# Kernel tuning notes

Measured on AMD Instinct MI355X. Metric: run time of the kernel, lower is better.

## Reference

```python
import jax, jax.numpy as jnp
import numpy as np

B, N, M = 2, 10000, 320000
F, LAT, STY = 64, 128, 128
HEADS, HID = 4, 32
OUT = 3 + F  # 67
NEG = 0.2    # leaky relu slope (both activation and GAT attention)
EPS = 1e-5


def leaky(x):
    return jax.nn.leaky_relu(x, NEG)


def layer_norm(x, g, b):
    mu = jnp.mean(x, axis=-1, keepdims=True)
    var = jnp.var(x, axis=-1, keepdims=True)
    return (x - mu) * jax.lax.rsqrt(var + EPS) * g + b


def gat_conv(h, src, dst, W, a_src, a_dst, bias, heads, out_dim, n_nodes, concat):
    # h: [n, in]; W: [in, heads*out_dim]; a_*: [heads, out_dim]
    ht = (h @ W).reshape(n_nodes, heads, out_dim)
    al_s = jnp.einsum('nhd,hd->nh', ht, a_src)  # source contribution
    al_d = jnp.einsum('nhd,hd->nh', ht, a_dst)  # destination contribution
    e = leaky(al_s[src] + al_d[dst])            # [E, heads]
    emax = jax.ops.segment_max(e, dst, num_segments=n_nodes)
    ex = jnp.exp(e - emax[dst])
    denom = jax.ops.segment_sum(ex, dst, num_segments=n_nodes)
    alpha = ex / (denom[dst] + 1e-16)           # scatter-softmax over in-edges
    msg = ht[src] * alpha[:, :, None]           # [E, heads, out_dim]
    agg = jax.ops.segment_sum(msg, dst, num_segments=n_nodes)
    agg = agg.reshape(n_nodes, heads * out_dim) if concat else agg.mean(axis=1)
    return agg + bias


def setup_inputs():
    key = jax.random.key(0)
    ks = jax.random.split(key, 20)
    g = lambda i, sh, s=0.05: jax.random.normal(ks[i], sh, jnp.float32) * s
    d = {}
    d['z'] = g(0, (B, LAT), 1.0)
    d['x'] = g(1, (N, F), 1.0)
    d['pos'] = g(2, (N, 3), 1.0)
    d['edge_index'] = jax.random.randint(ks[3], (2, M), 0, N)
    d['w1'] = g(4, (LAT, 256)); d['b1'] = jnp.zeros((256,), jnp.float32)
    d['w2'] = g(5, (256, 512)); d['b2'] = jnp.zeros((512,), jnp.float32)
    d['w3'] = g(6, (512, STY)); d['b3'] = jnp.zeros((STY,), jnp.float32)
    in0 = F + STY
    d['gw0'] = g(7, (in0, HEADS * HID)); d['ga0s'] = g(8, (HEADS, HID)); d['ga0d'] = g(9, (HEADS, HID)); d['gb0'] = jnp.zeros((HEADS * HID,), jnp.float32)
    in1 = HEADS * HID
    d['gw1'] = g(10, (in1, HEADS * HID)); d['ga1s'] = g(11, (HEADS, HID)); d['ga1d'] = g(12, (HEADS, HID)); d['gb1'] = jnp.zeros((HEADS * HID,), jnp.float32)
    d['gw2'] = g(13, (in1, OUT)); d['ga2s'] = g(14, (1, OUT)); d['ga2d'] = g(15, (1, OUT)); d['gb2'] = jnp.zeros((OUT,), jnp.float32)
    d['ln0_g'] = jnp.ones((in1,), jnp.float32); d['ln0_b'] = jnp.zeros((in1,), jnp.float32)
    d['ln1_g'] = jnp.ones((in1,), jnp.float32); d['ln1_b'] = jnp.zeros((in1,), jnp.float32)
    return d


def _batched_edges(edge_index):
    # replicate template edges B times with node-id offsets, then add self-loops
    ei = jnp.concatenate([edge_index + b * N for b in range(B)], axis=1)
    sl = jnp.arange(B * N, dtype=edge_index.dtype)
    src = jnp.concatenate([ei[0], sl])
    dst = jnp.concatenate([ei[1], sl])
    return src, dst


def _forward(z, x, pos, src, dst,
             w1, b1, w2, b2, w3, b3,
             gw0, ga0s, ga0d, gb0, gw1, ga1s, ga1d, gb1, gw2, ga2s, ga2d, gb2,
             ln0_g, ln0_b, ln1_g, ln1_b):
    n_tot = B * N
    # style MLP
    s = leaky(z @ w1 + b1)
    s = leaky(s @ w2 + b2)
    style = s @ w3 + b3                               # [B, STY]
    xb = jnp.tile(x, (B, 1))                          # [B*N, F]
    pb = jnp.tile(pos, (B, 1))                        # [B*N, 3]
    style_exp = jnp.repeat(style, N, axis=0)          # [B*N, STY]
    H = jnp.concatenate([xb, style_exp], axis=1)
    H = gat_conv(H, src, dst, gw0, ga0s, ga0d, gb0, HEADS, HID, n_tot, True)
    H = leaky(layer_norm(H, ln0_g, ln0_b))
    H = gat_conv(H, src, dst, gw1, ga1s, ga1d, gb1, HEADS, HID, n_tot, True)
    H = leaky(layer_norm(H, ln1_g, ln1_b))
    H_out = gat_conv(H, src, dst, gw2, ga2s, ga2d, gb2, 1, OUT, n_tot, False)
    p_new = pb + H_out[:, :3]
    f_new = xb + H_out[:, 3:]
    return f_new, p_new


def reference(z, x, pos, edge_index,
              w1, b1, w2, b2, w3, b3,
              gw0, ga0s, ga0d, gb0, gw1, ga1s, ga1d, gb1, gw2, ga2s, ga2d, gb2,
              ln0_g, ln0_b, ln1_g, ln1_b):
    src, dst = _batched_edges(edge_index)
    return _forward(z, x, pos, src, dst,
                    w1, b1, w2, b2, w3, b3,
                    gw0, ga0s, ga0d, gb0, gw1, ga1s, ga1d, gb1, gw2, ga2s, ga2d, gb2,
                    ln0_g, ln0_b, ln1_g, ln1_b)
```

## Files before the change

kernel.cpp:

```cpp
#include <hip/hip_runtime.h>
#include <hip/hip_bf16.h>

#define DEV_INLINE __device__ __forceinline__

constexpr int Nn   = 10000;
constexpr int NT   = 20000;
constexpr int Me   = 320000;
constexpr int STRIDE = 96;
constexpr float NEG = 0.2f;

typedef float  f32x4  __attribute__((ext_vector_type(4)));
typedef float  f32x2  __attribute__((ext_vector_type(2)));
typedef short  bf16x8 __attribute__((ext_vector_type(8)));

DEV_INLINE float leaky(float x){ return x >= 0.f ? x : NEG*x; }

DEV_INLINE ushort f2bf(float v){
  __hip_bfloat16 h = __float2bfloat16(v);
  return *reinterpret_cast<ushort*>(&h);
}
DEV_INLINE float bf2f(ushort u){
  uint x = ((uint)u) << 16;
  return __uint_as_float(x);
}

DEV_INLINE unsigned char f2f8(float v){
#if __has_builtin(__builtin_amdgcn_cvt_pk_fp8_f32)
  return (unsigned char)(__builtin_amdgcn_cvt_pk_fp8_f32(v, v, 0, false) & 0xFF);
#else
  uint u = __float_as_uint(v);
  uint s = (u >> 24) & 0x80u;
  uint au = u & 0x7FFFFFFFu;
  if (au >= 0x43E00000u) return (unsigned char)(s | 0x7Eu);
  uint au2 = au + 0x0007FFFFu + ((au >> 20) & 1u);
  int e = (int)(au2 >> 23) - 120;
  if (e <= 0) return (unsigned char)s;
  uint r = ((uint)e << 3) | ((au2 >> 20) & 7u);
  if (r >= 0x7Fu) r = 0x7Eu;
  return (unsigned char)(s | r);
#endif
}
template<bool HI>
DEV_INLINE f32x2 f8x2f(uint p){
#if __has_builtin(__builtin_amdgcn_cvt_pk_f32_fp8)
  return __builtin_amdgcn_cvt_pk_f32_fp8((int)p, HI);
#else
  uint b0 = HI ? ((p >> 16) & 0xFFu) : (p & 0xFFu);
  uint b1 = HI ? ((p >> 24) & 0xFFu) : ((p >> 8) & 0xFFu);
  f32x2 r;
  uint m0 = b0 & 0x7Fu, m1 = b1 & 0x7Fu;
  uint f0 = (m0 >= 8) ? ((m0 + 960u) << 20) : 0u;
  uint f1 = (m1 >= 8) ? ((m1 + 960u) << 20) : 0u;
  f0 |= (b0 & 0x80u) << 24; f1 |= (b1 & 0x80u) << 24;
  r.x = __uint_as_float(f0); r.y = __uint_as_float(f1);
  return r;
#endif
}

DEV_INLINE float sel4(float4 w, int h){
  return h < 2 ? (h == 0 ? w.x : w.y) : (h == 2 ? w.z : w.w);
}
DEV_INLINE float red16(float v){
  v += __shfl_xor(v, 1); v += __shfl_xor(v, 2);
  v += __shfl_xor(v, 4); v += __shfl_xor(v, 8);
  return v;
}
DEV_INLINE float red32(float v){
  v += __shfl_xor(v, 1); v += __shfl_xor(v, 2);
  v += __shfl_xor(v, 4); v += __shfl_xor(v, 8);
  v += __shfl_xor(v, 16);
  return v;
}

template<int K>
__global__ __launch_bounds__(256) void k_mlp(const float* __restrict__ in,
    const float* __restrict__ W, const float* __restrict__ bias,
    float* __restrict__ out, int OD, int doAct, int mlpBlocks,
    int* __restrict__ zbuf, int zn, int zblk,
    const float* __restrict__ w3, const float* __restrict__ G,
    float* __restrict__ M, const float* __restrict__ b3, float* __restrict__ bG,
    int mblk){
  if ((int)blockIdx.x >= mlpBlocks){
    int b2 = blockIdx.x - mlpBlocks;
    if (b2 < zblk){
      int i = b2*256 + threadIdx.x;
      if (i < zn) zbuf[i] = 0;
    } else if ((b2 -= zblk) < mblk){
      int k = b2*2 + (threadIdx.x >> 7);
      int j = threadIdx.x & 127;
      float a = 0.f;
      for (int m=0; m<128; m++) a += w3[k*128 + m] * G[m*128 + j];
      M[(size_t)k*128 + j] = a;
    } else {
      if (threadIdx.x < 128){
        int j = threadIdx.x;
        float a = 0.f;
        for (int m=0; m<128; m++) a += b3[m] * G[m*128 + j];
        bG[j] = a;
      }
    }
    return;
  }
  int wave = threadIdx.x >> 6, lane = threadIdx.x & 63;
  int o = blockIdx.x*4 + wave;
  if (o >= 2*OD) return;
  int b = (o >= OD) ? 1 : 0;
  int j = o - b*OD;
  const float* __restrict__ ip = in + b*K;
  float acc = 0.f;
  #pragma unroll 2
  for (int k = lane; k < K; k += 64) acc += ip[k] * W[(size_t)k*OD + j];
  #pragma unroll
  for (int off = 32; off; off >>= 1) acc += __shfl_xor(acc, off);
  if (lane == 0){
    float v = acc + (bias ? bias[j] : 0.f);
    out[o] = doAct ? leaky(v) : v;
  }
}

__global__ __launch_bounds__(256) void k_ht0_mfma(const float* __restrict__ x,
    const float* __restrict__ gw0, const float* __restrict__ styleW0,
    const float* __restrict__ a_s, const float* __restrict__ a_d,
    unsigned char* __restrict__ ht0, float* __restrict__ alS, float* __restrict__ alD,
    int mbBlocks, const int* __restrict__ eidx, int* __restrict__ cnt,
    ushort* __restrict__ slot){
  if ((int)blockIdx.x >= mbBlocks){
    int e = (blockIdx.x - mbBlocks)*256 + threadIdx.x;
    if (e < Me){
      int s = eidx[e], d = eidx[Me + e];
      int p = atomicAdd(&cnt[d], 1);
      if (p < STRIDE) slot[(size_t)d*STRIDE + p] = (ushort)s;
    }
    return;
  }
  __shared__ ushort bt[128*64];
  __shared__ float stycS[2][4], stycD[2][4];
  int t = threadIdx.x;
  int lane = t & 63, l15 = lane & 15, g = lane >> 4;
  int wid = t >> 6;
  int mbase = blockIdx.x*128 + wid*32;

  bf16x8 afr[2][2];
  #pragma unroll
  for (int mf=0; mf<2; mf++){
    int row = mbase + mf*16 + l15;
    int rc = row < Nn ? row : Nn-1;
    const float* xp = x + (size_t)rc*64 + g*8;
    #pragma unroll
    for (int ks=0; ks<2; ks++){
      float4 va = *(const float4*)(xp + ks*32);
      float4 vb = *(const float4*)(xp + ks*32 + 4);
      bf16x8 f;
      f[0] = (short)f2bf(va.x); f[1] = (short)f2bf(va.y);
      f[2] = (short)f2bf(va.z); f[3] = (short)f2bf(va.w);
      f[4] = (short)f2bf(vb.x); f[5] = (short)f2bf(vb.y);
      f[6] = (short)f2bf(vb.z); f[7] = (short)f2bf(vb.w);
      afr[mf][ks] = f;
    }
  }

  for (int idx = t; idx < 64*128; idx += 256){
    int k = idx >> 7, c = idx & 127;
    uint byte = ((uint)(c*64 + k) << 1) ^ ((uint)(c&7) << 4);
    *(ushort*)((char*)bt + byte) = f2bf(gw0[k*128 + c]);
  }

  if (t < 128){
    int c = t, h = c >> 5;
    float as_c = a_s[c], ad_c = a_d[c];
    float s0 = styleW0[c], s1 = styleW0[128 + c];
    float v0s = red32(s0*as_c), v0d = red32(s0*ad_c);
    float v1s = red32(s1*as_c), v1d = red32(s1*ad_c);
    if ((lane & 31) == 0){
      stycS[0][h] = v0s; stycD[0][h] = v0d;
      stycS[1][h] = v1s; stycD[1][h] = v1d;
    }
  }
  __syncthreads();

  f32x4 acc[2][8];
  #pragma unroll
  for (int mf=0; mf<2; mf++)
    #pragma unroll
    for (int nf=0; nf<8; nf++) acc[mf][nf] = (f32x4){0.f,0.f,0.f,0.f};

  #pragma unroll
  for (int ks=0; ks<2; ks++){
    int kb = ks*32 + g*8;
    bf16x8 bfr[8];
    #pragma unroll
    for (int nf=0; nf<8; nf++){
      int c = nf*16 + l15;
      uint byte = ((uint)(c*64 + kb) << 1) ^ ((uint)(c&7) << 4);
      bfr[nf] = *(const bf16x8*)((const char*)bt + byte);
    }
    #pragma unroll
    for (int mf=0; mf<2; mf++)
      #pragma unroll
      for (int nf=0; nf<8; nf++)
        acc[mf][nf] = __builtin_amdgcn_mfma_f32_16x16x32_bf16(
            afr[mf][ks], bfr[nf], acc[mf][nf], 0, 0, 0);
  }

  float sw0[8], sw1[8], as_v[8], ad_v[8];
  #pragma unroll
  for (int nf=0; nf<8; nf++){
    int c = nf*16 + l15;
    sw0[nf] = styleW0[c]; sw1[nf] = styleW0[128 + c];
    as_v[nf] = a_s[c];    ad_v[nf] = a_d[c];
  }
  #pragma unroll
  for (int mf=0; mf<2; mf++){
    int rbase = mbase + mf*16 + g*4;
    #pragma unroll
    for (int r=0; r<4; r++){
      int row = rbase + r;
      bool ok = (row < Nn);
      #pragma unroll
      for (int nf=0; nf<8; nf++){
        int c = nf*16 + l15;
        if (ok){
          float v = acc[mf][nf][r];
          ht0[(size_t)row*128 + c]      = f2f8(v + sw0[nf]);
          ht0[(size_t)(Nn+row)*128 + c] = f2f8(v + sw1[nf]);
        }
      }
      float ps0 = acc[mf][0][r]*as_v[0] + acc[mf][1][r]*as_v[1];
      float ps1 = acc[mf][2][r]*as_v[2] + acc[mf][3][r]*as_v[3];
      float ps2 = acc[mf][4][r]*as_v[4] + acc[mf][5][r]*as_v[5];
      float ps3 = acc[mf][6][r]*as_v[6] + acc[mf][7][r]*as_v[7];
      float pd0 = acc[mf][0][r]*ad_v[0] + acc[mf][1][r]*ad_v[1];
      float pd1 = acc[mf][2][r]*ad_v[2] + acc[mf][3][r]*ad_v[3];
      float pd2 = acc[mf][4][r]*ad_v[4] + acc[mf][5][r]*ad_v[5];
      float pd3 = acc[mf][6][r]*ad_v[6] + acc[mf][7][r]*ad_v[7];
      ps0 = red16(ps0); ps1 = red16(ps1); ps2 = red16(ps2); ps3 = red16(ps3);
      pd0 = red16(pd0); pd1 = red16(pd1); pd2 = red16(pd2); pd3 = red16(pd3);
      if (l15 == 0 && ok){
        *(float4*)(alS + (size_t)row*4) = make_float4(
            ps0 + stycS[0][0], ps1 + stycS[0][1], ps2 + stycS[0][2], ps3 + stycS[0][3]);
        *(float4*)(alD + (size_t)row*4) = make_float4(
            pd0 + stycD[0][0], pd1 + stycD[0][1], pd2 + stycD[0][2], pd3 + stycD[0][3]);
        *(float4*)(alS + (size_t)(Nn+row)*4) = make_float4(
            ps0 + stycS[1][0], ps1 + stycS[1][1], ps2 + stycS[1][2], ps3 + stycS[1][3]);
        *(float4*)(alD + (size_t)(Nn+row)*4) = make_float4(
            pd0 + stycD[1][0], pd1 + stycD[1][1], pd2 + stycD[1][2], pd3 + stycD[1][3]);
      }
    }
  }
}

template<int NCOL, int LDO, int NF, int NHEAD>
__global__ __launch_bounds__(256) void k_mm_mfma(const ushort* __restrict__ A,
    const float* __restrict__ W, unsigned char* __restrict__ out,
    const float* __restrict__ a_s, const float* __restrict__ a_d,
    float* __restrict__ alS, float* __restrict__ alD, int M){
  constexpr int NCOLP = NF*16;
  __shared__ ushort bt[NCOLP*128];
  int t = threadIdx.x;
  int wid = t >> 6, lane = t & 63, l15 = lane & 15, g = lane >> 4;
  int mbase = blockIdx.x*128 + wid*32;

  bf16x8 afr[2][4];
  #pragma unroll
  for (int mf=0; mf<2; mf++){
    int row = mbase + mf*16 + l15;
    int rc = row < M ? row : M-1;
    const ushort* ap = A + (size_t)rc*128 + g*8;
    #pragma unroll
    for (int ks=0; ks<4; ks++)
      afr[mf][ks] = *(const bf16x8*)(ap + ks*32);
  }

  for (int idx = t; idx < 128*NCOLP; idx += 256){
    int k = idx / NCOLP, c = idx % NCOLP;
    float v = (c < NCOL) ? W[k*NCOL + c] : 0.f;
    uint byte = ((uint)(c*128 + k) << 1) ^ ((uint)(c&7) << 4);
    *(ushort*)((char*)bt + byte) = f2bf(v);
  }
  __syncthreads();

  f32x4 acc[2][NF];
  #pragma unroll
  for (int mf=0; mf<2; mf++)
    #pragma unroll
    for (int nf=0; nf<NF; nf++) acc[mf][nf] = (f32x4){0.f,0.f,0.f,0.f};

  #pragma unroll
  for (int ks=0; ks<4; ks++){
    int kb = ks*32 + g*8;
    bf16x8 bfr[NF];
    #pragma unroll
    for (int nf=0; nf<NF; nf++){
      int c = nf*16 + l15;
      uint byte = ((uint)(c*128 + kb) << 1) ^ ((uint)(c&7) << 4);
      bfr[nf] = *(const bf16x8*)((const char*)bt + byte);
    }
    #pragma unroll
    for (int mf=0; mf<2; mf++)
      #pragma unroll
      for (int nf=0; nf<NF; nf++)
        acc[mf][nf] = __builtin_amdgcn_mfma_f32_16x16x32_bf16(
            afr[mf][ks], bfr[nf], acc[mf][nf], 0, 0, 0);
  }

  #pragma unroll
  for (int mf=0; mf<2; mf++){
    int rbase = mbase + mf*16 + g*4;
    #pragma unroll
    for (int nf=0; nf<NF; nf++){
      int c = nf*16 + l15;
      if (c < LDO){
        #pragma unroll
        for (int r=0; r<4; r++){
          int row = rbase + r;
          if (row < M) out[(size_t)row*LDO + c] =
              (c < NCOL) ? f2f8(acc[mf][nf][r]) : (unsigned char)0;
        }
      }
    }
  }

  float as_v[NF], ad_v[NF];
  #pragma unroll
  for (int nf=0; nf<NF; nf++){
    int c = nf*16 + l15;
    as_v[nf] = (c < NCOL) ? a_s[c] : 0.f;
    ad_v[nf] = (c < NCOL) ? a_d[c] : 0.f;
  }
  #pragma unroll
  for (int mf=0; mf<2; mf++){
    #pragma unroll
    for (int r=0; r<4; r++){
      int row = mbase + mf*16 + g*4 + r;
      if constexpr (NHEAD == 4){
        float ps0 = acc[mf][0][r]*as_v[0] + acc[mf][1][r]*as_v[1];
        float ps1 = acc[mf][2][r]*as_v[2] + acc[mf][3][r]*as_v[3];
        float ps2 = acc[mf][4][r]*as_v[4] + acc[mf][5][r]*as_v[5];
        float ps3 = acc[mf][6][r]*as_v[6] + acc[mf][7][r]*as_v[7];
        float pd0 = acc[mf][0][r]*ad_v[0] + acc[mf][1][r]*ad_v[1];
        float pd1 = acc[mf][2][r]*ad_v[2] + acc[mf][3][r]*ad_v[3];
        float pd2 = acc[mf][4][r]*ad_v[4] + acc[mf][5][r]*ad_v[5];
        float pd3 = acc[mf][6][r]*ad_v[6] + acc[mf][7][r]*ad_v[7];
        ps0 = red16(ps0); ps1 = red16(ps1); ps2 = red16(ps2); ps3 = red16(ps3);
        pd0 = red16(pd0); pd1 = red16(pd1); pd2 = red16(pd2); pd3 = red16(pd3);
        if (l15 == 0 && row < M){
          *(float4*)(alS + (size_t)row*4) = make_float4(ps0, ps1, ps2, ps3);
          *(float4*)(alD + (size_t)row*4) = make_float4(pd0, pd1, pd2, pd3);
        }
      } else {
        float ps = 0.f, pd = 0.f;
        #pragma unroll
        for (int nf=0; nf<NF; nf++){
          ps += acc[mf][nf][r]*as_v[nf];
          pd += acc[mf][nf][r]*ad_v[nf];
        }
        ps = red16(ps); pd = red16(pd);
        if (l15 == 0 && row < M){
          alS[row] = ps; alD[row] = pd;
        }
      }
    }
  }
}

__global__ __launch_bounds__(256) void k_gat128(const unsigned char* __restrict__ ht,
    const float* __restrict__ alS, const float* __restrict__ alD,
    const int* __restrict__ deg, const ushort* __restrict__ slot,
    const float* __restrict__ gb, const float* __restrict__ lng,
    const float* __restrict__ lnb, ushort* __restrict__ outH, int n){
  __shared__ float wbuf[4][4][68];
  __shared__ int   sbuf[4][64];
  int wave = threadIdx.x >> 6, lane = threadIdx.x & 63;
  int dd = blockIdx.x*4 + wave;
  if (dd >= n) return;
  int tr  = (dd >= Nn) ? dd - Nn : dd;
  int off = (dd >= Nn) ? Nn : 0;
  int sub = lane >> 5, li = lane & 31;
  int c0 = li*4;
  int h  = li >> 3;
  float4 ald4 = *(const float4*)(alD + dd*4);
  int dg = deg[tr]; if (dg > STRIDE) dg = STRIDE;
  int begin = tr*STRIDE, end = begin + dg;

  float4 asl = *(const float4*)(alS + dd*4);
  float4 wsl;
  wsl.x = __expf(leaky(asl.x + ald4.x));
  wsl.y = __expf(leaky(asl.y + ald4.y));
  wsl.z = __expf(leaky(asl.z + ald4.z));
  wsl.w = __expf(leaky(asl.w + ald4.w));
  float es = sel4(wsl, h);
  float acc0=0.f, acc1=0.f, acc2=0.f, acc3=0.f, den=0.f;
  if (sub == 0){
    uint sv = *(const uint*)(ht + (size_t)dd*128 + c0);
    f32x2 lo = f8x2f<false>(sv), hi = f8x2f<true>(sv);
    den = es;
    acc0 = es * lo.x; acc1 = es * lo.y;
    acc2 = es * hi.x; acc3 = es * hi.y;
  }

  const unsigned char* __restrict__ htp = ht + c0;

  for (int j = begin; j < end; j += 64){
    int nc = min(64, end - j);
    if (lane < nc){
      int s = (int)slot[j + lane] + off;
      float4 as4 = *(const float4*)(alS + s*4);
      wbuf[wave][0][lane] = __expf(leaky(as4.x + ald4.x));
      wbuf[wave][1][lane] = __expf(leaky(as4.y + ald4.y));
      wbuf[wave][2][lane] = __expf(leaky(as4.z + ald4.z));
      wbuf[wave][3][lane] = __expf(leaky(as4.w + ald4.w));
      sbuf[wave][lane] = s;
    }
    const float* __restrict__ wh = wbuf[wave][h];
    int q = 0;
    for (; q + 8 <= nc; q += 8){
      int sv[4]; float wv[4];
      #pragma unroll
      for (int u=0;u<4;u++){ int e = q + 2*u + sub; sv[u] = sbuf[wave][e]; wv[u] = wh[e]; }
      uint hv[4];
      #pragma unroll
      for (int u=0;u<4;u++) hv[u] = *(const uint*)(htp + (size_t)sv[u]*128);
      #pragma unroll
      for (int u=0;u<4;u++){
        f32x2 lo = f8x2f<false>(hv[u]), hi = f8x2f<true>(hv[u]);
        den  += wv[u];
        acc0 += wv[u] * lo.x; acc1 += wv[u] * lo.y;
        acc2 += wv[u] * hi.x; acc3 += wv[u] * hi.y;
      }
    }
    for (; q < nc; q += 2){
      int e = q + sub;
      if (e < nc){
        int s = sbuf[wave][e];
        float w = wh[e];
        uint hv = *(const uint*)(htp + (size_t)s*128);
        f32x2 lo = f8x2f<false>(hv), hi = f8x2f<true>(hv);
        den  += w;
        acc0 += w * lo.x; acc1 += w * lo.y;
        acc2 += w * hi.x; acc3 += w * hi.y;
      }
    }
  }
  acc0 += __shfl_xor(acc0, 32); acc1 += __shfl_xor(acc1, 32);
  acc2 += __shfl_xor(acc2, 32); acc3 += __shfl_xor(acc3, 32);
  den  += __shfl_xor(den, 32);

  float idn = 1.f / (den + 1e-16f);
  float4 gbv = *(const float4*)(gb + c0);
  float v0 = acc0*idn + gbv.x;
  float v1 = acc1*idn + gbv.y;
  float v2 = acc2*idn + gbv.z;
  float v3 = acc3*idn + gbv.w;

  float sum = v0+v1+v2+v3;
  float sq  = v0*v0+v1*v1+v2*v2+v3*v3;
  sum = red32(sum); sq = red32(sq);
  float mu  = sum * (1.f/128.f);
  float var = sq  * (1.f/128.f) - mu*mu;
  float inv = rsqrtf(var + 1e-5f);
  float4 lg = *(const float4*)(lng + c0);
  float4 lb = *(const float4*)(lnb + c0);
  if (sub == 0){
    float y0 = (v0 - mu)*inv*lg.x + lb.x;
    float y1 = (v1 - mu)*inv*lg.y + lb.y;
    float y2 = (v2 - mu)*inv*lg.z + lb.z;
    float y3 = (v3 - mu)*inv*lg.w + lb.w;
    uint2 ow;
    ow.x = (uint)f2bf(leaky(y0)) | ((uint)f2bf(leaky(y1)) << 16);
    ow.y = (uint)f2bf(leaky(y2)) | ((uint)f2bf(leaky(y3)) << 16);
    *(uint2*)(outH + (size_t)dd*128 + c0) = ow;
  }
}

__global__ __launch_bounds__(256) void k_gat_out(const unsigned char* __restrict__ ht2,
    const float* __restrict__ alS, const float* __restrict__ alD,
    const int* __restrict__ deg, const ushort* __restrict__ slot,
    const float* __restrict__ gb2, const float* __restrict__ x,
    const float* __restrict__ pos, float* __restrict__ out, int n){
  __shared__ float wbuf[4][64];
  __shared__ int   sbuf[4][64];
  int wave = threadIdx.x >> 6, lane = threadIdx.x & 63;
  int dd = blockIdx.x*4 + wave;
  if (dd >= n) return;
  int tr  = (dd >= Nn) ? dd - Nn : dd;
  int off = (dd >= Nn) ? Nn : 0;
  int c0 = lane*2;
  bool act = (c0 < 67);
  float ald = alD[dd];
  int dg = deg[tr]; if (dg > STRIDE) dg = STRIDE;
  int begin = tr*STRIDE, end = begin + dg;

  float wsl = __expf(leaky(alS[dd] + ald));
  float den  = wsl;
  uint sv0 = act ? (uint)*(const ushort*)(ht2 + (size_t)dd*68 + c0) : 0u;
  f32x2 sd = f8x2f<false>(sv0);
  float acc0 = wsl * sd.x;
  float acc1 = wsl * sd.y;

  const unsigned char* __restrict__ h2p = ht2 + c0;

  for (int j = begin; j < end; j += 64){
    int nc = min(64, end - j);
    if (lane < nc){
      int s = (int)slot[j + lane] + off;
      wbuf[wave][lane] = __expf(leaky(alS[s] + ald));
      sbuf[wave][lane] = s;
    }
    int q = 0;
    for (; q + 8 <= nc; q += 8){
      int sv[8]; float wv[8];
      #pragma unroll
      for (int u=0;u<8;u++){ sv[u] = sbuf[wave][q+u]; wv[u] = wbuf[wave][q+u]; }
      uint hv[8];
      #pragma unroll
      for (int u=0;u<8;u++) hv[u] = act ? (uint)*(const ushort*)(h2p + (size_t)sv[u]*68) : 0u;
      #pragma unroll
      for (int u=0;u<8;u++){
        f32x2 d = f8x2f<false>(hv[u]);
        den  += wv[u];
        acc0 += wv[u] * d.x;
        acc1 += wv[u] * d.y;
      }
    }
    for (; q < nc; q++){
      int s = sbuf[wave][q]; float w = wbuf[wave][q];
      uint hv = act ? (uint)*(const ushort*)(h2p + (size_t)s*68) : 0u;
      f32x2 d = f8x2f<false>(hv);
      den  += w;
      acc0 += w * d.x;
      acc1 += w * d.y;
    }
  }
  if (!act) return;
  float idn = 1.f / (den + 1e-16f);
  int i = tr;
  int c1 = c0 + 1;
  float v0 = acc0*idn + gb2[c0];
  if (c0 < 3) out[NT*64 + dd*3 + c0] = pos[i*3 + c0] + v0;
  else        out[dd*64 + (c0-3)]    = x[i*64 + (c0-3)] + v0;
  if (c1 < 67){
    float v1 = acc1*idn + gb2[c1];
    if (c1 < 3) out[NT*64 + dd*3 + c1] = pos[i*3 + c1] + v1;
    else        out[dd*64 + (c1-3)]    = x[i*64 + (c1-3)] + v1;
  }
}

extern "C" void kernel_launch(void* const* d_in, const int* in_sizes, int n_in,
                              void* d_out, int out_size, void* d_ws, size_t ws_size,
                              hipStream_t stream){
  const float* z    = (const float*)d_in[0];
  const float* x    = (const float*)d_in[1];
  const float* pos  = (const float*)d_in[2];
  const int*   eidx = (const int*)  d_in[3];
  const float* w1   = (const float*)d_in[4];
  const float* b1   = (const float*)d_in[5];
  const float* w2   = (const float*)d_in[6];
  const float* b2   = (const float*)d_in[7];
  const float* w3   = (const float*)d_in[8];
  const float* b3   = (const float*)d_in[9];
  const float* gw0  = (const float*)d_in[10];
  const float* ga0s = (const float*)d_in[11];
  const float* ga0d = (const float*)d_in[12];
  const float* gb0  = (const float*)d_in[13];
  const float* gw1  = (const float*)d_in[14];
  const float* ga1s = (const float*)d_in[15];
  const float* ga1d = (const float*)d_in[16];
  const float* gb1  = (const float*)d_in[17];
  const float* gw2  = (const float*)d_in[18];
  const float* ga2s = (const float*)d_in[19];
  const float* ga2d = (const float*)d_in[20];
  const float* gb2  = (const float*)d_in[21];
  const float* ln0g = (const float*)d_in[22];
  const float* ln0b = (const float*)d_in[23];
  const float* ln1g = (const float*)d_in[24];
  const float* ln1b = (const float*)d_in[25];
  float* out = (float*)d_out;

  float* ws       = (float*)d_ws;
  float* styleW0  = ws;
  float* s1buf    = ws + 256;
  float* s2buf    = s1buf + 512;
  float* Mbuf     = s2buf + 1024;
  float* bGbuf    = Mbuf + 512*128;
  float* alS      = bGbuf + 128;
  float* alD      = alS + 80000;
  unsigned char* htA = (unsigned char*)(alD + 80000);
  ushort* htB     = (ushort*)(htA + (size_t)NT*128);
  unsigned char* ht2c = (unsigned char*)(htB + (size_t)NT*128);
  int*   cnt      = (int*)(ht2c + (size_t)NT*68);
  ushort* slot    = (ushort*)(cnt + Nn);

  const float* G = gw0 + 64*128;

  const int ZB  = (Nn + 255)/256;
  const int MBk = 256;
  k_mlp<128><<<128 + ZB + MBk + 1, 256, 0, stream>>>(
      z, w1, b1, s1buf, 256, 1, 128,
      cnt, Nn, ZB, w3, G, Mbuf, b3, bGbuf, MBk);
  k_mlp<256><<<256, 256, 0, stream>>>(s1buf, w2, b2, s2buf, 512, 1, 256,
      nullptr, 0, 0, nullptr, nullptr, nullptr, nullptr, nullptr, 0);
  k_mlp<512><<<64, 256, 0, stream>>>(s2buf, Mbuf, bGbuf, styleW0, 128, 0, 64,
      nullptr, 0, 0, nullptr, nullptr, nullptr, nullptr, nullptr, 0);

  const int MB0 = (Nn+127)/128;
  const int EB  = (Me+255)/256;
  k_ht0_mfma<<<MB0 + EB, 256, 0, stream>>>(x, gw0, styleW0, ga0s, ga0d,
                                           htA, alS, alD, MB0, eidx, cnt, slot);
  k_gat128<<<(NT+3)/4, 256, 0, stream>>>(htA, alS, alD, cnt, slot,
                                         gb0, ln0g, ln0b, htB, NT);
  const int MB = (NT+127)/128;
  k_mm_mfma<128,128,8,4><<<MB, 256, 0, stream>>>(htB, gw1, htA, ga1s, ga1d, alS, alD, NT);
  k_gat128<<<(NT+3)/4, 256, 0, stream>>>(htA, alS, alD, cnt, slot,
                                         gb1, ln1g, ln1b, htB, NT);
  k_mm_mfma<67,68,5,1><<<MB, 256, 0, stream>>>(htB, gw2, ht2c, ga2s, ga2d, alS, alD, NT);
  k_gat_out<<<(NT+3)/4, 256, 0, stream>>>(ht2c, alS, alD, cnt, slot,
                                          gb2, x, pos, out, NT);
}
```

Before: 130.3 us.

## Process both batch copies of each node per wave in GAT aggregation kernels

```diff
diff --git a/kernel.cpp b/kernel.cpp
--- a/kernel.cpp
+++ b/kernel.cpp
@@ -367,35 +367,37 @@
     const float* __restrict__ alS, const float* __restrict__ alD,
     const int* __restrict__ deg, const ushort* __restrict__ slot,
     const float* __restrict__ gb, const float* __restrict__ lng,
-    const float* __restrict__ lnb, ushort* __restrict__ outH, int n){
-  __shared__ float wbuf[4][4][68];
+    const float* __restrict__ lnb, ushort* __restrict__ outH){
+  __shared__ float wbuf[4][8][68];
   __shared__ int   sbuf[4][64];
   int wave = threadIdx.x >> 6, lane = threadIdx.x & 63;
-  int dd = blockIdx.x*4 + wave;
-  if (dd >= n) return;
-  int tr  = (dd >= Nn) ? dd - Nn : dd;
-  int off = (dd >= Nn) ? Nn : 0;
+  int tr = blockIdx.x*4 + wave;
+  if (tr >= Nn) return;
   int sub = lane >> 5, li = lane & 31;
   int c0 = li*4;
   int h  = li >> 3;
-  float4 ald4 = *(const float4*)(alD + dd*4);
+  float4 ad0 = *(const float4*)(alD + (size_t)tr*4);
+  float4 ad1 = *(const float4*)(alD + (size_t)(tr+Nn)*4);
   int dg = deg[tr]; if (dg > STRIDE) dg = STRIDE;
   int begin = tr*STRIDE, end = begin + dg;
 
-  float4 asl = *(const float4*)(alS + dd*4);
-  float4 wsl;
-  wsl.x = __expf(leaky(asl.x + ald4.x));
-  wsl.y = __expf(leaky(asl.y + ald4.y));
-  wsl.z = __expf(leaky(asl.z + ald4.z));
-  wsl.w = __expf(leaky(asl.w + ald4.w));
-  float es = sel4(wsl, h);
-  float acc0=0.f, acc1=0.f, acc2=0.f, acc3=0.f, den=0.f;
+  float4 as0 = *(const float4*)(alS + (size_t)tr*4);
+  float4 as1 = *(const float4*)(alS + (size_t)(tr+Nn)*4);
+  float4 w0s, w1s;
+  w0s.x = __expf(leaky(as0.x + ad0.x)); w0s.y = __expf(leaky(as0.y + ad0.y));
+  w0s.z = __expf(leaky(as0.z + ad0.z)); w0s.w = __expf(leaky(as0.w + ad0.w));
+  w1s.x = __expf(leaky(as1.x + ad1.x)); w1s.y = __expf(leaky(as1.y + ad1.y));
+  w1s.z = __expf(leaky(as1.z + ad1.z)); w1s.w = __expf(leaky(as1.w + ad1.w));
+  float e0s = sel4(w0s, h), e1s = sel4(w1s, h);
+  float a00=0,a01=0,a02=0,a03=0,den0=0;
+  float a10=0,a11=0,a12=0,a13=0,den1=0;
   if (sub == 0){
-    uint sv = *(const uint*)(ht + (size_t)dd*128 + c0);
-    f32x2 lo = f8x2f<false>(sv), hi = f8x2f<true>(sv);
-    den = es;
-    acc0 = es * lo.x; acc1 = es * lo.y;
-    acc2 = es * hi.x; acc3 = es * hi.y;
+    uint v0 = *(const uint*)(ht + (size_t)tr*128 + c0);
+    uint v1 = *(const uint*)(ht + (size_t)(tr+Nn)*128 + c0);
+    f32x2 l0 = f8x2f<false>(v0), h0v = f8x2f<true>(v0);
+    f32x2 l1 = f8x2f<false>(v1), h1v = f8x2f<true>(v1);
+    den0 = e0s; a00 = e0s*l0.x; a01 = e0s*l0.y; a02 = e0s*h0v.x; a03 = e0s*h0v.y;
+    den1 = e1s; a10 = e1s*l1.x; a11 = e1s*l1.y; a12 = e1s*h1v.x; a13 = e1s*h1v.y;
   }
 
   const unsigned char* __restrict__ htp = ht + c0;
@@ -403,72 +405,105 @@
   for (int j = begin; j < end; j += 64){
     int nc = min(64, end - j);
     if (lane < nc){
-      int s = (int)slot[j + lane] + off;
-      float4 as4 = *(const float4*)(alS + s*4);
-      wbuf[wave][0][lane] = __expf(leaky(as4.x + ald4.x));
-      wbuf[wave][1][lane] = __expf(leaky(as4.y + ald4.y));
-      wbuf[wave][2][lane] = __expf(leaky(as4.z + ald4.z));
-      wbuf[wave][3][lane] = __expf(leaky(as4.w + ald4.w));
+      int s = (int)slot[j + lane];
+      float4 p0 = *(const float4*)(alS + (size_t)s*4);
+      float4 p1 = *(const float4*)(alS + (size_t)(s+Nn)*4);
+      wbuf[wave][0][lane] = __expf(leaky(p0.x + ad0.x));
+      wbuf[wave][1][lane] = __expf(leaky(p0.y + ad0.y));
+      wbuf[wave][2][lane] = __expf(leaky(p0.z + ad0.z));
+      wbuf[wave][3][lane] = __expf(leaky(p0.w + ad0.w));
+      wbuf[wave][4][lane] = __expf(leaky(p1.x + ad1.x));
+      wbuf[wave][5][lane] = __expf(leaky(p1.y + ad1.y));
+      wbuf[wave][6][lane] = __expf(leaky(p1.z + ad1.z));
+      wbuf[wave][7][lane] = __expf(leaky(p1.w + ad1.w));
       sbuf[wave][lane] = s;
     }
-    const float* __restrict__ wh = wbuf[wave][h];
+    const float* __restrict__ wh0 = wbuf[wave][h];
+    const float* __restrict__ wh1 = wbuf[wave][4+h];
     int q = 0;
     for (; q + 8 <= nc; q += 8){
-      int sv[4]; float wv[4];
-      #pragma unroll
-      for (int u=0;u<4;u++){ int e = q + 2*u + sub; sv[u] = sbuf[wave][e]; wv[u] = wh[e]; }
-      uint hv[4];
-      #pragma unroll
-      for (int u=0;u<4;u++) hv[u] = *(const uint*)(htp + (size_t)sv[u]*128);
+      int sv[4]; float v0[4], v1[4];
+      #pragma unroll
+      for (int u=0;u<4;u++){ int e = q + 2*u + sub; sv[u] = sbuf[wave][e]; v0[u] = wh0[e]; v1[u] = wh1[e]; }
+      uint g0[4], g1[4];
       #pragma unroll
       for (int u=0;u<4;u++){
-        f32x2 lo = f8x2f<false>(hv[u]), hi = f8x2f<true>(hv[u]);
-        den  += wv[u];
-        acc0 += wv[u] * lo.x; acc1 += wv[u] * lo.y;
-        acc2 += wv[u] * hi.x; acc3 += wv[u] * hi.y;
+        g0[u] = *(const uint*)(htp + (size_t)sv[u]*128);
+        g1[u] = *(const uint*)(htp + ((size_t)sv[u]+Nn)*128);
+      }
+      #pragma unroll
+      for (int u=0;u<4;u++){
+        f32x2 lo0 = f8x2f<false>(g0[u]), hi0 = f8x2f<true>(g0[u]);
+        f32x2 lo1 = f8x2f<false>(g1[u]), hi1 = f8x2f<true>(g1[u]);
+        den0 += v0[u];
+        a00 += v0[u]*lo0.x; a01 += v0[u]*lo0.y; a02 += v0[u]*hi0.x; a03 += v0[u]*hi0.y;
+        den1 += v1[u];
+        a10 += v1[u]*lo1.x; a11 += v1[u]*lo1.y; a12 += v1[u]*hi1.x; a13 += v1[u]*hi1.y;
       }
     }
     for (; q < nc; q += 2){
       int e = q + sub;
       if (e < nc){
         int s = sbuf[wave][e];
-        float w = wh[e];
-        uint hv = *(const uint*)(htp + (size_t)s*128);
-        f32x2 lo = f8x2f<false>(hv), hi = f8x2f<true>(hv);
-        den  += w;
-        acc0 += w * lo.x; acc1 += w * lo.y;
-        acc2 += w * hi.x; acc3 += w * hi.y;
-      }
-    }
-  }
-  acc0 += __shfl_xor(acc0, 32); acc1 += __shfl_xor(acc1, 32);
-  acc2 += __shfl_xor(acc2, 32); acc3 += __shfl_xor(acc3, 32);
-  den  += __shfl_xor(den, 32);
-
-  float idn = 1.f / (den + 1e-16f);
+        float v0 = wh0[e], v1 = wh1[e];
+        uint g0 = *(const uint*)(htp + (size_t)s*128);
+        uint g1 = *(const uint*)(htp + ((size_t)s+Nn)*128);
+        f32x2 lo0 = f8x2f<false>(g0), hi0 = f8x2f<true>(g0);
+        f32x2 lo1 = f8x2f<false>(g1), hi1 = f8x2f<true>(g1);
+        den0 += v0; a00 += v0*lo0.x; a01 += v0*lo0.y; a02 += v0*hi0.x; a03 += v0*hi0.y;
+        den1 += v1; a10 += v1*lo1.x; a11 += v1*lo1.y; a12 += v1*hi1.x; a13 += v1*hi1.y;
+      }
+    }
+  }
+  a00 += __shfl_xor(a00, 32); a01 += __shfl_xor(a01, 32);
+  a02 += __shfl_xor(a02, 32); a03 += __shfl_xor(a03, 32);
+  a10 += __shfl_xor(a10, 32); a11 += __shfl_xor(a11, 32);
+  a12 += __shfl_xor(a12, 32); a13 += __shfl_xor(a13, 32);
+  den0 += __shfl_xor(den0, 32); den1 += __shfl_xor(den1, 32);
+
   float4 gbv = *(const float4*)(gb + c0);
-  float v0 = acc0*idn + gbv.x;
-  float v1 = acc1*idn + gbv.y;
-  float v2 = acc2*idn + gbv.z;
-  float v3 = acc3*idn + gbv.w;
-
-  float sum = v0+v1+v2+v3;
-  float sq  = v0*v0+v1*v1+v2*v2+v3*v3;
-  sum = red32(sum); sq = red32(sq);
-  float mu  = sum * (1.f/128.f);
-  float var = sq  * (1.f/128.f) - mu*mu;
-  float inv = rsqrtf(var + 1e-5f);
   float4 lg = *(const float4*)(lng + c0);
   float4 lb = *(const float4*)(lnb + c0);
-  if (sub == 0){
-    float y0 = (v0 - mu)*inv*lg.x + lb.x;
-    float y1 = (v1 - mu)*inv*lg.y + lb.y;
-    float y2 = (v2 - mu)*inv*lg.z + lb.z;
-    float y3 = (v3 - mu)*inv*lg.w + lb.w;
-    uint2 ow;
-    ow.x = (uint)f2bf(leaky(y0)) | ((uint)f2bf(leaky(y1)) << 16);
-    ow.y = (uint)f2bf(leaky(y2)) | ((uint)f2bf(leaky(y3)) << 16);
-    *(uint2*)(outH + (size_t)dd*128 + c0) = ow;
+
+  {
+    float idn = 1.f / (den0 + 1e-16f);
+    float v0 = a00*idn + gbv.x, v1 = a01*idn + gbv.y;
+    float v2 = a02*idn + gbv.z, v3 = a03*idn + gbv.w;
+    float sum = red32(v0+v1+v2+v3);
+    float sq  = red32(v0*v0+v1*v1+v2*v2+v3*v3);
+    float mu  = sum * (1.f/128.f);
+    float var = sq  * (1.f/128.f) - mu*mu;
+    float inv = rsqrtf(var + 1e-5f);
+    if (sub == 0){
+      float y0 = (v0 - mu)*inv*lg.x + lb.x;
+      float y1 = (v1 - mu)*inv*lg.y + lb.y;
+      float y2 = (v2 - mu)*inv*lg.z + lb.z;
+      float y3 = (v3 - mu)*inv*lg.w + lb.w;
+      uint2 ow;
+      ow.x = (uint)f2bf(leaky(y0)) | ((uint)f2bf(leaky(y1)) << 16);
+      ow.y = (uint)f2bf(leaky(y2)) | ((uint)f2bf(leaky(y3)) << 16);
+      *(uint2*)(outH + (size_t)tr*128 + c0) = ow;
+    }
+  }
+  {
+    float idn = 1.f / (den1 + 1e-16f);
+    float v0 = a10*idn + gbv.x, v1 = a11*idn + gbv.y;
+    float v2 = a12*idn + gbv.z, v3 = a13*idn + gbv.w;
+    float sum = red32(v0+v1+v2+v3);
+    float sq  = red32(v0*v0+v1*v1+v2*v2+v3*v3);
+    float mu  = sum * (1.f/128.f);
+    float var = sq  * (1.f/128.f) - mu*mu;
+    float inv = rsqrtf(var + 1e-5f);
+    if (sub == 0){
+      float y0 = (v0 - mu)*inv*lg.x + lb.x;
+      float y1 = (v1 - mu)*inv*lg.y + lb.y;
+      float y2 = (v2 - mu)*inv*lg.z + lb.z;
+      float y3 = (v3 - mu)*inv*lg.w + lb.w;
+      uint2 ow;
+      ow.x = (uint)f2bf(leaky(y0)) | ((uint)f2bf(leaky(y1)) << 16);
+      ow.y = (uint)f2bf(leaky(y2)) | ((uint)f2bf(leaky(y3)) << 16);
+      *(uint2*)(outH + (size_t)(tr+Nn)*128 + c0) = ow;
+    }
   }
 }
 
@@ -476,72 +511,89 @@
     const float* __restrict__ alS, const float* __restrict__ alD,
     const int* __restrict__ deg, const ushort* __restrict__ slot,
     const float* __restrict__ gb2, const float* __restrict__ x,
-    const float* __restrict__ pos, float* __restrict__ out, int n){
-  __shared__ float wbuf[4][64];
+    const float* __restrict__ pos, float* __restrict__ out){
+  __shared__ float wbuf[4][2][64];
   __shared__ int   sbuf[4][64];
   int wave = threadIdx.x >> 6, lane = threadIdx.x & 63;
-  int dd = blockIdx.x*4 + wave;
-  if (dd >= n) return;
-  int tr  = (dd >= Nn) ? dd - Nn : dd;
-  int off = (dd >= Nn) ? Nn : 0;
+  int tr = blockIdx.x*4 + wave;
+  if (tr >= Nn) return;
   int c0 = lane*2;
   bool act = (c0 < 67);
-  float ald = alD[dd];
+  float ald0 = alD[tr], ald1 = alD[tr+Nn];
   int dg = deg[tr]; if (dg > STRIDE) dg = STRIDE;
   int begin = tr*STRIDE, end = begin + dg;
 
-  float wsl = __expf(leaky(alS[dd] + ald));
-  float den  = wsl;
-  uint sv0 = act ? (uint)*(const ushort*)(ht2 + (size_t)dd*68 + c0) : 0u;
-  f32x2 sd = f8x2f<false>(sv0);
-  float acc0 = wsl * sd.x;
-  float acc1 = wsl * sd.y;
+  float w0s = __expf(leaky(alS[tr] + ald0));
+  float w1s = __expf(leaky(alS[tr+Nn] + ald1));
+  float den0 = w0s, den1 = w1s;
+  uint v0i = act ? (uint)*(const ushort*)(ht2 + (size_t)tr*68 + c0) : 0u;
+  uint v1i = act ? (uint)*(const ushort*)(ht2 + (size_t)(tr+Nn)*68 + c0) : 0u;
+  f32x2 s0 = f8x2f<false>(v0i), s1 = f8x2f<false>(v1i);
+  float a00 = w0s*s0.x, a01 = w0s*s0.y;
+  float a10 = w1s*s1.x, a11 = w1s*s1.y;
 
   const unsigned char* __restrict__ h2p = ht2 + c0;
 
   for (int j = begin; j < end; j += 64){
     int nc = min(64, end - j);
     if (lane < nc){
-      int s = (int)slot[j + lane] + off;
-      wbuf[wave][lane] = __expf(leaky(alS[s] + ald));
+      int s = (int)slot[j + lane];
+      wbuf[wave][0][lane] = __expf(leaky(alS[s] + ald0));
+      wbuf[wave][1][lane] = __expf(leaky(alS[s+Nn] + ald1));
       sbuf[wave][lane] = s;
     }
     int q = 0;
-    for (; q + 8 <= nc; q += 8){
-      int sv[8]; float wv[8];
-      #pragma unroll
-      for (int u=0;u<8;u++){ sv[u] = sbuf[wave][q+u]; wv[u] = wbuf[wave][q+u]; }
-      uint hv[8];
-      #pragma unroll
-      for (int u=0;u<8;u++) hv[u] = act ? (uint)*(const ushort*)(h2p + (size_t)sv[u]*68) : 0u;
-      #pragma unroll
-      for (int u=0;u<8;u++){
-        f32x2 d = f8x2f<false>(hv[u]);
-        den  += wv[u];
-        acc0 += wv[u] * d.x;
-        acc1 += wv[u] * d.y;
+    for (; q + 4 <= nc; q += 4){
+      int sv[4]; float v0[4], v1[4];
+      #pragma unroll
+      for (int u=0;u<4;u++){ sv[u] = sbuf[wave][q+u]; v0[u] = wbuf[wave][0][q+u]; v1[u] = wbuf[wave][1][q+u]; }
+      uint g0[4], g1[4];
+      #pragma unroll
+      for (int u=0;u<4;u++){
+        g0[u] = act ? (uint)*(const ushort*)(h2p + (size_t)sv[u]*68) : 0u;
+        g1[u] = act ? (uint)*(const ushort*)(h2p + ((size_t)sv[u]+Nn)*68) : 0u;
+      }
+      #pragma unroll
+      for (int u=0;u<4;u++){
+        f32x2 d0 = f8x2f<false>(g0[u]), d1 = f8x2f<false>(g1[u]);
+        den0 += v0[u]; a00 += v0[u]*d0.x; a01 += v0[u]*d0.y;
+        den1 += v1[u]; a10 += v1[u]*d1.x; a11 += v1[u]*d1.y;
       }
     }
     for (; q < nc; q++){
-      int s = sbuf[wave][q]; float w = wbuf[wave][q];
-      uint hv = act ? (uint)*(const ushort*)(h2p + (size_t)s*68) : 0u;
-      f32x2 d = f8x2f<false>(hv);
-      den  += w;
-      acc0 += w * d.x;
-      acc1 += w * d.y;
+      int s = sbuf[wave][q];
+      float v0 = wbuf[wave][0][q], v1 = wbuf[wave][1][q];
+      uint g0 = act ? (uint)*(const ushort*)(h2p + (size_t)s*68) : 0u;
+      uint g1 = act ? (uint)*(const ushort*)(h2p + ((size_t)s+Nn)*68) : 0u;
+      f32x2 d0 = f8x2f<false>(g0), d1 = f8x2f<false>(g1);
+      den0 += v0; a00 += v0*d0.x; a01 += v0*d0.y;
+      den1 += v1; a10 += v1*d1.x; a11 += v1*d1.y;
     }
   }
   if (!act) return;
-  float idn = 1.f / (den + 1e-16f);
-  int i = tr;
-  int c1 = c0 + 1;
-  float v0 = acc0*idn + gb2[c0];
-  if (c0 < 3) out[NT*64 + dd*3 + c0] = pos[i*3 + c0] + v0;
-  else        out[dd*64 + (c0-3)]    = x[i*64 + (c0-3)] + v0;
-  if (c1 < 67){
-    float v1 = acc1*idn + gb2[c1];
-    if (c1 < 3) out[NT*64 + dd*3 + c1] = pos[i*3 + c1] + v1;
-    else        out[dd*64 + (c1-3)]    = x[i*64 + (c1-3)] + v1;
+  int i = tr, c1 = c0 + 1;
+  {
+    float idn = 1.f / (den0 + 1e-16f);
+    float v0 = a00*idn + gb2[c0];
+    if (c0 < 3) out[NT*64 + tr*3 + c0] = pos[i*3 + c0] + v0;
+    else        out[(size_t)tr*64 + (c0-3)] = x[i*64 + (c0-3)] + v0;
+    if (c1 < 67){
+      float v1 = a01*idn + gb2[c1];
+      if (c1 < 3) out[NT*64 + tr*3 + c1] = pos[i*3 + c1] + v1;
+      else        out[(size_t)tr*64 + (c1-3)] = x[i*64 + (c1-3)] + v1;
+    }
+  }
+  {
+    int dd = tr + Nn;
+    float idn = 1.f / (den1 + 1e-16f);
+    float v0 = a10*idn + gb2[c0];
+    if (c0 < 3) out[NT*64 + dd*3 + c0] = pos[i*3 + c0] + v0;
+    else        out[(size_t)dd*64 + (c0-3)] = x[i*64 + (c0-3)] + v0;
+    if (c1 < 67){
+      float v1 = a11*idn + gb2[c1];
+      if (c1 < 3) out[NT*64 + dd*3 + c1] = pos[i*3 + c1] + v1;
+      else        out[(size_t)dd*64 + (c1-3)] = x[i*64 + (c1-3)] + v1;
+    }
   }
 }
 
@@ -606,13 +658,13 @@
   const int EB  = (Me+255)/256;
   k_ht0_mfma<<<MB0 + EB, 256, 0, stream>>>(x, gw0, styleW0, ga0s, ga0d,
                                            htA, alS, alD, MB0, eidx, cnt, slot);
-  k_gat128<<<(NT+3)/4, 256, 0, stream>>>(htA, alS, alD, cnt, slot,
-                                         gb0, ln0g, ln0b, htB, NT);
+  k_gat128<<<(Nn+3)/4, 256, 0, stream>>>(htA, alS, alD, cnt, slot,
+                                         gb0, ln0g, ln0b, htB);
   const int MB = (NT+127)/128;
   k_mm_mfma<128,128,8,4><<<MB, 256, 0, stream>>>(htB, gw1, htA, ga1s, ga1d, alS, alD, NT);
-  k_gat128<<<(NT+3)/4, 256, 0, stream>>>(htA, alS, alD, cnt, slot,
-                                         gb1, ln1g, ln1b, htB, NT);
+  k_gat128<<<(Nn+3)/4, 256, 0, stream>>>(htA, alS, alD, cnt, slot,
+                                         gb1, ln1g, ln1b, htB);
   k_mm_mfma<67,68,5,1><<<MB, 256, 0, stream>>>(htB, gw2, ht2c, ga2s, ga2d, alS, alD, NT);
-  k_gat_out<<<(NT+3)/4, 256, 0, stream>>>(ht2c, alS, alD, cnt, slot,
-                                          gb2, x, pos, out, NT);
-}
+  k_gat_out<<<(Nn+3)/4, 256, 0, stream>>>(ht2c, alS, alD, cnt, slot,
+                                          gb2, x, pos, out);
+}
```

Result: no change. 132.5 us (+1.7%).
